# Kernel tuning notes

Hardware: AMD Instinct MI355X
Metric: run time of the kernel (lower is better)

## Reference

```python
import jax, jax.numpy as jnp
import numpy as np

IN_DIM = 2048


def setup_inputs() -> dict:
    key = jax.random.key(0)
    ks = jax.random.split(key, 7)
    s = 1.0 / np.sqrt(IN_DIM)
    x = jax.random.normal(ks[0], (8, 256, IN_DIM), dtype=jnp.float32)
    Wq = jax.random.uniform(ks[1], (IN_DIM, IN_DIM), jnp.float32, -s, s)
    bq = jax.random.uniform(ks[2], (IN_DIM,), jnp.float32, -s, s)
    Wk = jax.random.uniform(ks[3], (IN_DIM, IN_DIM), jnp.float32, -s, s)
    bk = jax.random.uniform(ks[4], (IN_DIM,), jnp.float32, -s, s)
    Wv = jax.random.uniform(ks[5], (IN_DIM, IN_DIM), jnp.float32, -s, s)
    bv = jax.random.uniform(ks[6], (IN_DIM,), jnp.float32, -s, s)
    return {"x": x, "Wq": Wq, "bq": bq, "Wk": Wk, "bk": bk, "Wv": Wv, "bv": bv}


def reference(x, Wq, bq, Wk, bk, Wv, bv):
    # x: [B, C, L]; Linear acts on last (L) axis; torch Linear: y = x @ W^T + b
    scale = 1.0 / jnp.sqrt(jnp.asarray(x.shape[-1], x.dtype))
    q = jnp.einsum('bcl,ml->bcm', x, Wq) + bq
    k = jnp.einsum('bcl,ml->bcm', x, Wk) + bk
    v = jnp.einsum('bcl,ml->bcm', x, Wv) + bv
    # attn[b,l,m] = sum_c q[b,c,l] * k[b,c,m]
    attn = jnp.einsum('bcl,bcm->blm', q, k) * scale  # [B, L, L]
    attn = jax.nn.softmax(attn, axis=-1)
    # out[b,c,l] = sum_m v[b,c,m] * attn[b,l,m]
    out = jnp.einsum('bcm,blm->bcl', v, attn)  # [B, C, L]
    return out
```

## Files before the change

### kernel.cpp

```cpp
#include <hip/hip_runtime.h>
#include <hip/hip_bf16.h>
#include <cstdint>
#include <cstddef>


typedef __bf16 bf16_t;
typedef __bf16 bf16x8 __attribute__((ext_vector_type(8)));
typedef __bf16 bf16x4 __attribute__((ext_vector_type(4)));
typedef float floatx4 __attribute__((ext_vector_type(4)));

#define GLD_LDS16(gptr, lptr)                                                  \
  __builtin_amdgcn_global_load_lds(                                            \
      (const __attribute__((address_space(1))) void*)(gptr),                   \
      (__attribute__((address_space(3))) void*)(lptr), 16, 0, 0)

__global__ __launch_bounds__(256) void cvt4_f32_bf16(
    const float* __restrict__ s0, const float* __restrict__ s1,
    const float* __restrict__ s2, const float* __restrict__ s3,
    bf16_t* __restrict__ d0, bf16_t* __restrict__ d1,
    bf16_t* __restrict__ d2, bf16_t* __restrict__ d3) {
  const float* s;
  bf16_t* d;
  switch (blockIdx.y) {
    case 0: s = s0; d = d0; break;
    case 1: s = s1; d = d1; break;
    case 2: s = s2; d = d2; break;
    default: s = s3; d = d3; break;
  }
  const int i = (blockIdx.x * 256 + threadIdx.x) * 4;
  const float4 v = *reinterpret_cast<const float4*>(s + i);
  bf16x4 o;
  o[0] = (bf16_t)v.x; o[1] = (bf16_t)v.y; o[2] = (bf16_t)v.z; o[3] = (bf16_t)v.w;
  *reinterpret_cast<bf16x4*>(d + i) = o;
}

__global__ __launch_bounds__(256) void gemm_bt(
    const bf16_t* __restrict__ Abase, const bf16_t* __restrict__ Bbase,
    bf16_t* __restrict__ Cbase, const float* __restrict__ biasBase, int K,
    int lda, int ldb, int ldc, long bsA, long bsB, long bsC, int bsBias) {
  __shared__ __align__(16) bf16_t lds_a[128 * 32];
  __shared__ __align__(16) bf16_t lds_b[128 * 32];

  const int tid = threadIdx.x;
  const int lane = tid & 63;
  const int wid = tid >> 6;
  const int brow = blockIdx.x * 128;
  const int bcol = blockIdx.y * 128;
  const int wr = wid >> 1, wc = wid & 1;

  const bf16_t* A = Abase + (long)blockIdx.z * bsA;
  const bf16_t* B = Bbase + (long)blockIdx.z * bsB;

  floatx4 acc[4][4];
#pragma unroll
  for (int m = 0; m < 4; m++)
#pragma unroll
    for (int n = 0; n < 4; n++) acc[m][n] = (floatx4)0.f;

  const int c0 = wid * 2, c1 = wid * 2 + 1;
  const int srow0 = c0 * 16 + (lane >> 2);
  const int srow1 = c1 * 16 + (lane >> 2);
  const int skoff = (lane & 3) * 8;

  for (int kk = 0; kk < K; kk += 32) {
    GLD_LDS16(A + (size_t)(brow + srow0) * lda + kk + skoff, lds_a + c0 * 512);
    GLD_LDS16(A + (size_t)(brow + srow1) * lda + kk + skoff, lds_a + c1 * 512);
    GLD_LDS16(B + (size_t)(bcol + srow0) * ldb + kk + skoff, lds_b + c0 * 512);
    GLD_LDS16(B + (size_t)(bcol + srow1) * ldb + kk + skoff, lds_b + c1 * 512);
    __syncthreads();

    bf16x8 af[4], bfr[4];
#pragma unroll
    for (int m = 0; m < 4; m++)
      af[m] = *(const bf16x8*)&lds_a[(wr * 64 + m * 16 + (lane & 15)) * 32 +
                                     (lane >> 4) * 8];
#pragma unroll
    for (int n = 0; n < 4; n++)
      bfr[n] = *(const bf16x8*)&lds_b[(wc * 64 + n * 16 + (lane & 15)) * 32 +
                                      (lane >> 4) * 8];
#pragma unroll
    for (int m = 0; m < 4; m++)
#pragma unroll
      for (int n = 0; n < 4; n++)
        acc[m][n] =
            __builtin_amdgcn_mfma_f32_16x16x32_bf16(af[m], bfr[n], acc[m][n], 0, 0, 0);
    __syncthreads();
  }

  const int r0 = (lane >> 4) * 4;
  const int cc = lane & 15;
  bf16_t* Cb = Cbase + (long)blockIdx.z * bsC;
  const float* bias = biasBase + (long)blockIdx.z * bsBias;

#pragma unroll
  for (int n = 0; n < 4; n++) {
    const int gj = bcol + wc * 64 + n * 16 + cc;
    const float badd = bias[gj];
#pragma unroll
    for (int m = 0; m < 4; m++) {
      const int gi = brow + wr * 64 + m * 16 + r0;
#pragma unroll
      for (int r = 0; r < 4; r++)
        Cb[(size_t)(gi + r) * ldc + gj] = (bf16_t)(acc[m][n][r] + badd);
    }
  }
}

__global__ __launch_bounds__(256) void transpose2k(const bf16_t* __restrict__ inb,
                                                   bf16_t* __restrict__ outb) {
  __shared__ bf16_t t[64][65];
  const bf16_t* in = inb + (long)blockIdx.z * (4l * 1024 * 1024);
  bf16_t* out = outb + (long)blockIdx.z * (4l * 1024 * 1024);
  const int bx = blockIdx.x * 64, by = blockIdx.y * 64;
  const int tx = threadIdx.x, ty = threadIdx.y;
  for (int r = ty; r < 64; r += 4)
    t[r][tx] = in[(size_t)(by + r) * 2048 + bx + tx];
  __syncthreads();
  for (int r = ty; r < 64; r += 4)
    out[(size_t)(bx + r) * 2048 + by + tx] = t[tx][r];
}

__global__ __launch_bounds__(512, 2) void flash3(
    const bf16_t* __restrict__ qT, const bf16_t* __restrict__ kT,
    const bf16_t* __restrict__ v, float* __restrict__ po,
    float* __restrict__ pl) {
  __shared__ __align__(16) bf16_t Ks[8192];
  __shared__ __align__(16) bf16_t Vs[8192];
  __shared__ __align__(16) bf16_t Ps[8 * 1280];

  const int tid = threadIdx.x, lane = tid & 63, w = tid >> 6;
  const int idx = blockIdx.x;
  const int b = idx & 7, sg = (idx >> 3) & 3, qt = idx >> 5;
  const int l0 = qt * 256;
  const int key0 = sg * 512;
  const int i15 = lane & 15, g4 = lane >> 4;

  const bf16_t* Qg = qT + (size_t)(l0 + w * 32) * 2048 + b * 256;
  const bf16_t* Kg = kT + (size_t)key0 * 2048 + b * 256;
  const bf16_t* Vg = v + (size_t)b * 256 * 2048 + key0;

  bf16x8 af0[8], af1[8];
#pragma unroll
  for (int ks = 0; ks < 8; ks++) {
    af0[ks] = *(const bf16x8*)&Qg[(size_t)i15 * 2048 + ks * 32 + g4 * 8];
    af1[ks] = *(const bf16x8*)&Qg[(size_t)(16 + i15) * 2048 + ks * 32 + g4 * 8];
  }

  const int srow = lane >> 2;
  const int sslot = (lane & 3) ^ ((lane >> 3) & 3);
  auto stageK = [&](const bf16_t* g) {
#pragma unroll
    for (int j = 0; j < 2; j++) {
      const int ch = w * 2 + j, ks = ch >> 1, mseg = ch & 1;
      GLD_LDS16(g + (size_t)(mseg * 16 + srow) * 2048 + ks * 32 + sslot * 8,
                Ks + ch * 512);
    }
  };
  auto stageV = [&](const bf16_t* g) {
#pragma unroll
    for (int j = 0; j < 2; j++) {
      const int ch = w * 2 + j;
      GLD_LDS16(g + (size_t)(ch * 16 + srow) * 2048 + sslot * 8, Vs + ch * 512);
    }
  };

  floatx4 acc_o0[16], acc_o1[16];
#pragma unroll
  for (int cf = 0; cf < 16; cf++) {
    acc_o0[cf] = (floatx4)0.f;
    acc_o1[cf] = (floatx4)0.f;
  }
  floatx4 acc_l0 = (floatx4)0.f, acc_l1 = (floatx4)0.f;

  bf16x8 vones;
#pragma unroll
  for (int j = 0; j < 8; j++) vones[j] = (bf16_t)1.0f;

  const float SC = 0.031880107f;
  const int slotr = g4 ^ ((i15 >> 1) & 3);

  stageK(Kg);
  stageV(Vg);
  __syncthreads();

  for (int t = 0; t < 16; t++) {
    floatx4 s00 = (floatx4)0.f, s01 = (floatx4)0.f;
    floatx4 s10 = (floatx4)0.f, s11 = (floatx4)0.f;
#pragma unroll
    for (int ks = 0; ks < 8; ks++) {
      const bf16x8 b0 = *(const bf16x8*)&Ks[ks * 1024 + i15 * 32 + slotr * 8];
      const bf16x8 b1 =
          *(const bf16x8*)&Ks[ks * 1024 + (16 + i15) * 32 + slotr * 8];
      s00 = __builtin_amdgcn_mfma_f32_16x16x32_bf16(af0[ks], b0, s00, 0, 0, 0);
      s01 = __builtin_amdgcn_mfma_f32_16x16x32_bf16(af0[ks], b1, s01, 0, 0, 0);
      s10 = __builtin_amdgcn_mfma_f32_16x16x32_bf16(af1[ks], b0, s10, 0, 0, 0);
      s11 = __builtin_amdgcn_mfma_f32_16x16x32_bf16(af1[ks], b1, s11, 0, 0, 0);
    }
    __syncthreads();
    if (t < 15) stageK(Kg + (size_t)(t + 1) * 32 * 2048);

    bf16_t* Pw = Ps + w * 1280;
#pragma unroll
    for (int r = 0; r < 4; r++) {
      Pw[(g4 * 4 + r) * 40 + i15] = (bf16_t)exp2f(s00[r] * SC);
      Pw[(g4 * 4 + r) * 40 + 16 + i15] = (bf16_t)exp2f(s01[r] * SC);
      Pw[(16 + g4 * 4 + r) * 40 + i15] = (bf16_t)exp2f(s10[r] * SC);
      Pw[(16 + g4 * 4 + r) * 40 + 16 + i15] = (bf16_t)exp2f(s11[r] * SC);
    }
    const bf16x8 pa0 = *(const bf16x8*)&Pw[i15 * 40 + g4 * 8];
    const bf16x8 pa1 = *(const bf16x8*)&Pw[(16 + i15) * 40 + g4 * 8];
    acc_l0 = __builtin_amdgcn_mfma_f32_16x16x32_bf16(pa0, vones, acc_l0, 0, 0, 0);
    acc_l1 = __builtin_amdgcn_mfma_f32_16x16x32_bf16(pa1, vones, acc_l1, 0, 0, 0);
#pragma unroll
    for (int cf = 0; cf < 16; cf++) {
      const bf16x8 bv = *(const bf16x8*)&Vs[(cf * 16 + i15) * 32 + slotr * 8];
      acc_o0[cf] = __builtin_amdgcn_mfma_f32_16x16x32_bf16(pa0, bv, acc_o0[cf], 0, 0, 0);
      acc_o1[cf] = __builtin_amdgcn_mfma_f32_16x16x32_bf16(pa1, bv, acc_o1[cf], 0, 0, 0);
    }
    __syncthreads();
    if (t < 15) stageV(Vg + (t + 1) * 32);
  }

  float* pob = po + ((size_t)(b * 4 + sg) * 2048 + l0 + w * 32) * 256;
#pragma unroll
  for (int cf = 0; cf < 16; cf++)
#pragma unroll
    for (int r = 0; r < 4; r++) {
      pob[(size_t)(g4 * 4 + r) * 256 + cf * 16 + i15] = acc_o0[cf][r];
      pob[(size_t)(16 + g4 * 4 + r) * 256 + cf * 16 + i15] = acc_o1[cf][r];
    }
  if (i15 == 0) {
    float* plb = pl + (size_t)(b * 4 + sg) * 2048 + l0 + w * 32;
#pragma unroll
    for (int r = 0; r < 4; r++) {
      plb[g4 * 4 + r] = acc_l0[r];
      plb[16 + g4 * 4 + r] = acc_l1[r];
    }
  }
}

__global__ __launch_bounds__(256) void combine4(
    const float* __restrict__ po, const float* __restrict__ pl,
    float* __restrict__ out) {
  __shared__ float invd[32];
  __shared__ float tile[32][33];
  const int lt = blockIdx.x, ct = blockIdx.y, b = blockIdx.z;
  const int l0 = lt * 32, c0 = ct * 32;
  const int t = threadIdx.x;

  if (t < 32) {
    float d = 0.f;
#pragma unroll
    for (int s = 0; s < 4; s++) d += pl[(size_t)(b * 4 + s) * 2048 + l0 + t];
    invd[t] = 1.f / d;
  }
  __syncthreads();

  const int c = t & 31;
#pragma unroll
  for (int pass = 0; pass < 4; pass++) {
    const int l = pass * 8 + (t >> 5);
    float acc = 0.f;
#pragma unroll
    for (int s = 0; s < 4; s++)
      acc += po[((size_t)(b * 4 + s) * 2048 + l0 + l) * 256 + c0 + c];
    tile[c][l] = acc * invd[l];
  }
  __syncthreads();

  const int oc = t >> 3, lw = (t & 7) * 4;
  float4 val = {tile[oc][lw], tile[oc][lw + 1], tile[oc][lw + 2], tile[oc][lw + 3]};
  *(float4*)&out[((size_t)b * 256 + c0 + oc) * 2048 + l0 + lw] = val;
}

extern "C" void kernel_launch(void* const* d_in, const int* in_sizes, int n_in,
                              void* d_out, int out_size, void* d_ws,
                              size_t ws_size, hipStream_t stream) {
  const float* x = (const float*)d_in[0];
  float* out = (float*)d_out;

  constexpr long M4 = 4l * 1024 * 1024;
  bf16_t* ws = (bf16_t*)d_ws;
  bf16_t* xb = ws;
  bf16_t* Wb = ws + M4;
  bf16_t* qkv = ws + 4 * M4;
  bf16_t* tT = ws + 7 * M4;
  float* po = (float*)(ws + 9 * M4);
  float* pl = po + 8l * 4 * 2048 * 256;
  float* biasw = pl + 8 * 4 * 2048;

  cvt4_f32_bf16<<<dim3(4096, 4), 256, 0, stream>>>(
      x, (const float*)d_in[1], (const float*)d_in[3], (const float*)d_in[5],
      xb, Wb, Wb + M4, Wb + 2 * M4);
  hipMemcpyAsync(biasw, d_in[2], 2048 * 4, hipMemcpyDeviceToDevice, stream);
  hipMemcpyAsync(biasw + 2048, d_in[4], 2048 * 4, hipMemcpyDeviceToDevice, stream);
  hipMemcpyAsync(biasw + 4096, d_in[6], 2048 * 4, hipMemcpyDeviceToDevice, stream);

  gemm_bt<<<dim3(16, 16, 3), 256, 0, stream>>>(
      xb, Wb, qkv, biasw, 2048, 2048, 2048, 2048, 0l, M4, M4, 2048);
  transpose2k<<<dim3(32, 32, 2), dim3(64, 4), 0, stream>>>(qkv, tT);
  flash3<<<dim3(256), 512, 0, stream>>>(tT, tT + M4, qkv + 2 * M4, po, pl);
  combine4<<<dim3(64, 8, 8), 256, 0, stream>>>(po, pl, out);
}
```

Measured before the change: 257.3 us.

## Fuse Q/K transpose into GEMM epilogue, halve flash block, store partials in fp16

The QKV GEMM now writes Q and K directly in transposed layout with vectorized bf16x4 stores and reads the biases straight from the inputs. This removes the separate transpose kernel and the three bias memcpys. The flash kernel moves to 256-thread blocks covering 128 query rows, launched as 512 blocks, with each wave staging more K/V chunks. Partial outputs are stored as fp16 instead of fp32 to halve the traffic between flash and combine, at some cost in precision.

```diff
diff --git a/kernel.cpp b/kernel.cpp
--- a/kernel.cpp
+++ b/kernel.cpp
@@ -5,6 +5,7 @@
 
 
 typedef __bf16 bf16_t;
+typedef _Float16 fp16_t;
 typedef __bf16 bf16x8 __attribute__((ext_vector_type(8)));
 typedef __bf16 bf16x4 __attribute__((ext_vector_type(4)));
 typedef float floatx4 __attribute__((ext_vector_type(4)));
@@ -34,22 +35,25 @@
   *reinterpret_cast<bf16x4*>(d + i) = o;
 }
 
-__global__ __launch_bounds__(256) void gemm_bt(
-    const bf16_t* __restrict__ Abase, const bf16_t* __restrict__ Bbase,
-    bf16_t* __restrict__ Cbase, const float* __restrict__ biasBase, int K,
-    int lda, int ldb, int ldc, long bsA, long bsB, long bsC, int bsBias) {
+__global__ __launch_bounds__(256) void gemm_qkv(
+    const bf16_t* __restrict__ xb, const bf16_t* __restrict__ Wball,
+    bf16_t* __restrict__ tT, bf16_t* __restrict__ vb,
+    const float* __restrict__ bq, const float* __restrict__ bk,
+    const float* __restrict__ bv) {
   __shared__ __align__(16) bf16_t lds_a[128 * 32];
   __shared__ __align__(16) bf16_t lds_b[128 * 32];
 
+  constexpr long M4 = 4l * 1024 * 1024;
   const int tid = threadIdx.x;
   const int lane = tid & 63;
   const int wid = tid >> 6;
   const int brow = blockIdx.x * 128;
   const int bcol = blockIdx.y * 128;
   const int wr = wid >> 1, wc = wid & 1;
-
-  const bf16_t* A = Abase + (long)blockIdx.z * bsA;
-  const bf16_t* B = Bbase + (long)blockIdx.z * bsB;
+  const int z = blockIdx.z;
+
+  const bf16_t* A = xb;
+  const bf16_t* B = Wball + (long)z * M4;
 
   floatx4 acc[4][4];
 #pragma unroll
@@ -62,11 +66,11 @@
   const int srow1 = c1 * 16 + (lane >> 2);
   const int skoff = (lane & 3) * 8;
 
-  for (int kk = 0; kk < K; kk += 32) {
-    GLD_LDS16(A + (size_t)(brow + srow0) * lda + kk + skoff, lds_a + c0 * 512);
-    GLD_LDS16(A + (size_t)(brow + srow1) * lda + kk + skoff, lds_a + c1 * 512);
-    GLD_LDS16(B + (size_t)(bcol + srow0) * ldb + kk + skoff, lds_b + c0 * 512);
-    GLD_LDS16(B + (size_t)(bcol + srow1) * ldb + kk + skoff, lds_b + c1 * 512);
+  for (int kk = 0; kk < 2048; kk += 32) {
+    GLD_LDS16(A + (size_t)(brow + srow0) * 2048 + kk + skoff, lds_a + c0 * 512);
+    GLD_LDS16(A + (size_t)(brow + srow1) * 2048 + kk + skoff, lds_a + c1 * 512);
+    GLD_LDS16(B + (size_t)(bcol + srow0) * 2048 + kk + skoff, lds_b + c0 * 512);
+    GLD_LDS16(B + (size_t)(bcol + srow1) * 2048 + kk + skoff, lds_b + c1 * 512);
     __syncthreads();
 
     bf16x8 af[4], bfr[4];
@@ -89,49 +93,52 @@
 
   const int r0 = (lane >> 4) * 4;
   const int cc = lane & 15;
-  bf16_t* Cb = Cbase + (long)blockIdx.z * bsC;
-  const float* bias = biasBase + (long)blockIdx.z * bsBias;
-
-#pragma unroll
-  for (int n = 0; n < 4; n++) {
-    const int gj = bcol + wc * 64 + n * 16 + cc;
-    const float badd = bias[gj];
-#pragma unroll
-    for (int m = 0; m < 4; m++) {
-      const int gi = brow + wr * 64 + m * 16 + r0;
-#pragma unroll
-      for (int r = 0; r < 4; r++)
-        Cb[(size_t)(gi + r) * ldc + gj] = (bf16_t)(acc[m][n][r] + badd);
-    }
-  }
-}
-
-__global__ __launch_bounds__(256) void transpose2k(const bf16_t* __restrict__ inb,
-                                                   bf16_t* __restrict__ outb) {
-  __shared__ bf16_t t[64][65];
-  const bf16_t* in = inb + (long)blockIdx.z * (4l * 1024 * 1024);
-  bf16_t* out = outb + (long)blockIdx.z * (4l * 1024 * 1024);
-  const int bx = blockIdx.x * 64, by = blockIdx.y * 64;
-  const int tx = threadIdx.x, ty = threadIdx.y;
-  for (int r = ty; r < 64; r += 4)
-    t[r][tx] = in[(size_t)(by + r) * 2048 + bx + tx];
-  __syncthreads();
-  for (int r = ty; r < 64; r += 4)
-    out[(size_t)(bx + r) * 2048 + by + tx] = t[tx][r];
-}
-
-__global__ __launch_bounds__(512, 2) void flash3(
+  const float* bias = (z == 0) ? bq : (z == 1) ? bk : bv;
+
+  if (z < 2) {
+    bf16_t* C = tT + (long)z * M4;
+#pragma unroll
+    for (int n = 0; n < 4; n++) {
+      const int gj = bcol + wc * 64 + n * 16 + cc;
+      const float badd = bias[gj];
+#pragma unroll
+      for (int m = 0; m < 4; m++) {
+        const int gi = brow + wr * 64 + m * 16 + r0;
+        bf16x4 o;
+#pragma unroll
+        for (int r = 0; r < 4; r++) o[r] = (bf16_t)(acc[m][n][r] + badd);
+        *(bf16x4*)&C[(size_t)gj * 2048 + gi] = o;
+      }
+    }
+  } else {
+    bf16_t* C = vb;
+#pragma unroll
+    for (int n = 0; n < 4; n++) {
+      const int gj = bcol + wc * 64 + n * 16 + cc;
+      const float badd = bias[gj];
+#pragma unroll
+      for (int m = 0; m < 4; m++) {
+        const int gi = brow + wr * 64 + m * 16 + r0;
+#pragma unroll
+        for (int r = 0; r < 4; r++)
+          C[(size_t)(gi + r) * 2048 + gj] = (bf16_t)(acc[m][n][r] + badd);
+      }
+    }
+  }
+}
+
+__global__ __launch_bounds__(256, 2) void flash3(
     const bf16_t* __restrict__ qT, const bf16_t* __restrict__ kT,
-    const bf16_t* __restrict__ v, float* __restrict__ po,
+    const bf16_t* __restrict__ v, fp16_t* __restrict__ po,
     float* __restrict__ pl) {
   __shared__ __align__(16) bf16_t Ks[8192];
   __shared__ __align__(16) bf16_t Vs[8192];
-  __shared__ __align__(16) bf16_t Ps[8 * 1280];
+  __shared__ __align__(16) bf16_t Ps[4 * 1280];
 
   const int tid = threadIdx.x, lane = tid & 63, w = tid >> 6;
   const int idx = blockIdx.x;
   const int b = idx & 7, sg = (idx >> 3) & 3, qt = idx >> 5;
-  const int l0 = qt * 256;
+  const int l0 = qt * 128;
   const int key0 = sg * 512;
   const int i15 = lane & 15, g4 = lane >> 4;
 
@@ -150,16 +157,16 @@
   const int sslot = (lane & 3) ^ ((lane >> 3) & 3);
   auto stageK = [&](const bf16_t* g) {
 #pragma unroll
-    for (int j = 0; j < 2; j++) {
-      const int ch = w * 2 + j, ks = ch >> 1, mseg = ch & 1;
+    for (int j = 0; j < 4; j++) {
+      const int ch = w * 4 + j, ks = ch >> 1, mseg = ch & 1;
       GLD_LDS16(g + (size_t)(mseg * 16 + srow) * 2048 + ks * 32 + sslot * 8,
                 Ks + ch * 512);
     }
   };
   auto stageV = [&](const bf16_t* g) {
 #pragma unroll
-    for (int j = 0; j < 2; j++) {
-      const int ch = w * 2 + j;
+    for (int j = 0; j < 4; j++) {
+      const int ch = w * 4 + j;
       GLD_LDS16(g + (size_t)(ch * 16 + srow) * 2048 + sslot * 8, Vs + ch * 512);
     }
   };
@@ -221,13 +228,14 @@
     if (t < 15) stageV(Vg + (t + 1) * 32);
   }
 
-  float* pob = po + ((size_t)(b * 4 + sg) * 2048 + l0 + w * 32) * 256;
+  fp16_t* pob = po + ((size_t)(b * 4 + sg) * 2048 + l0 + w * 32) * 256;
 #pragma unroll
   for (int cf = 0; cf < 16; cf++)
 #pragma unroll
     for (int r = 0; r < 4; r++) {
-      pob[(size_t)(g4 * 4 + r) * 256 + cf * 16 + i15] = acc_o0[cf][r];
-      pob[(size_t)(16 + g4 * 4 + r) * 256 + cf * 16 + i15] = acc_o1[cf][r];
+      pob[(size_t)(g4 * 4 + r) * 256 + cf * 16 + i15] = (fp16_t)acc_o0[cf][r];
+      pob[(size_t)(16 + g4 * 4 + r) * 256 + cf * 16 + i15] =
+          (fp16_t)acc_o1[cf][r];
     }
   if (i15 == 0) {
     float* plb = pl + (size_t)(b * 4 + sg) * 2048 + l0 + w * 32;
@@ -240,7 +248,7 @@
 }
 
 __global__ __launch_bounds__(256) void combine4(
-    const float* __restrict__ po, const float* __restrict__ pl,
+    const fp16_t* __restrict__ po, const float* __restrict__ pl,
     float* __restrict__ out) {
   __shared__ float invd[32];
   __shared__ float tile[32][33];
@@ -263,7 +271,7 @@
     float acc = 0.f;
 #pragma unroll
     for (int s = 0; s < 4; s++)
-      acc += po[((size_t)(b * 4 + s) * 2048 + l0 + l) * 256 + c0 + c];
+      acc += (float)po[((size_t)(b * 4 + s) * 2048 + l0 + l) * 256 + c0 + c];
     tile[c][l] = acc * invd[l];
   }
   __syncthreads();
@@ -283,22 +291,20 @@
   bf16_t* ws = (bf16_t*)d_ws;
   bf16_t* xb = ws;
   bf16_t* Wb = ws + M4;
-  bf16_t* qkv = ws + 4 * M4;
-  bf16_t* tT = ws + 7 * M4;
-  float* po = (float*)(ws + 9 * M4);
-  float* pl = po + 8l * 4 * 2048 * 256;
-  float* biasw = pl + 8 * 4 * 2048;
+  bf16_t* tT = ws + 4 * M4;
+  bf16_t* vb = ws + 6 * M4;
+  fp16_t* po = (fp16_t*)(ws + 7 * M4);
+  float* pl = (float*)(po + 8l * 4 * 2048 * 256);
 
   cvt4_f32_bf16<<<dim3(4096, 4), 256, 0, stream>>>(
       x, (const float*)d_in[1], (const float*)d_in[3], (const float*)d_in[5],
       xb, Wb, Wb + M4, Wb + 2 * M4);
-  hipMemcpyAsync(biasw, d_in[2], 2048 * 4, hipMemcpyDeviceToDevice, stream);
-  hipMemcpyAsync(biasw + 2048, d_in[4], 2048 * 4, hipMemcpyDeviceToDevice, stream);
-  hipMemcpyAsync(biasw + 4096, d_in[6], 2048 * 4, hipMemcpyDeviceToDevice, stream);
-
-  gemm_bt<<<dim3(16, 16, 3), 256, 0, stream>>>(
-      xb, Wb, qkv, biasw, 2048, 2048, 2048, 2048, 0l, M4, M4, 2048);
-  transpose2k<<<dim3(32, 32, 2), dim3(64, 4), 0, stream>>>(qkv, tT);
-  flash3<<<dim3(256), 512, 0, stream>>>(tT, tT + M4, qkv + 2 * M4, po, pl);
+
+  gemm_qkv<<<dim3(16, 16, 3), 256, 0, stream>>>(
+      xb, Wb, tT, vb, (const float*)d_in[2], (const float*)d_in[4],
+      (const float*)d_in[6]);
+
+  flash3<<<dim3(512), 256, 0, stream>>>(tT, tT + M4, vb, po, pl);
+
   combine4<<<dim3(64, 8, 8), 256, 0, stream>>>(po, pl, out);
 }
```

New measurement: 228.2 us. 11.3% less time.
